# Optimization experiments

Measured on AMD Instinct MI355X. Metric: run time of the kernel, lower is better.

Reference implementation:

```python
import jax, jax.numpy as jnp
import numpy as np

B, C, H, W = 2, 128, 256, 256
E = 2                      # expan_att_chans
NUM_CHANS = 4
HEADS = NUM_CHANS * E      # 8
D = C // NUM_CHANS         # 32 head dim
EPS = 1e-12


def setup_inputs() -> dict:
    key = jax.random.key(0)
    ks = jax.random.split(key, 6)
    s = 0.05
    return {
        "x": jax.random.normal(ks[0], (B, C, H, W), jnp.float32),
        "w_qkv": jax.random.normal(ks[1], (C, 3 * E), jnp.float32) * s,   # groups=C, 1->3E per group
        "b_qkv": jax.random.normal(ks[2], (C, 3 * E), jnp.float32) * s,
        "w_fus": jax.random.normal(ks[3], (C, E), jnp.float32) * s,       # groups=C, E->1 per group
        "b_fus": jax.random.normal(ks[4], (C,), jnp.float32) * s,
        "t": jnp.ones((1, HEADS, 1, 1), jnp.float32),                     # learned temperature
    }


def _l2norm(a):
    n = jnp.sqrt(jnp.sum(a * a, axis=-1, keepdims=True))
    return a / jnp.maximum(n, EPS)


def reference(x, w_qkv, b_qkv, w_fus, b_fus, t):
    Bs, Cs, Hs, Ws = x.shape
    HW = Hs * Ws
    # grouped 1x1 conv (groups=C): each input channel -> 3E outputs
    qkv = jnp.einsum('bchw,ce->bechw', x, w_qkv) + b_qkv.T[None, :, :, None, None]
    # qkv: [B, 3E, C, H, W]; chunk into q,k,v along dim 1
    q, k, v = qkv[:, :E], qkv[:, E:2 * E], qkv[:, 2 * E:]
    # [B, E, C, H, W] -> [B, heads, d, HW]
    q = q.reshape(Bs, HEADS, D, HW)
    k = k.reshape(Bs, HEADS, D, HW)
    v = v.reshape(Bs, HEADS, D, HW)
    q = _l2norm(q)
    k = _l2norm(k)
    attn = jnp.einsum('bhdn,bhen->bhde', q, k) * t   # [B, heads, d, d]
    attn = jax.nn.softmax(attn, axis=-1)
    o = jnp.einsum('bhde,bhen->bhdn', attn, v)       # [B, heads, d, HW]
    # [B, heads, d, HW] -> [B, E, C, H, W] -> [B, C, E, H, W]
    o = o.reshape(Bs, E, Cs, Hs, Ws).transpose(0, 2, 1, 3, 4)
    # grouped 1x1 conv (groups=C): E inputs -> 1 output per channel
    out = jnp.einsum('bcehw,ce->bchw', o, w_fus) + b_fus[None, :, None, None]
    return out
```

## Files before the change

### kernel.cpp

```cpp
#include <hip/hip_runtime.h>
#include <hip/hip_bf16.h>
#include <cmath>

typedef __bf16 bf16_t;
typedef __attribute__((ext_vector_type(8)))  __bf16 bf16x8;
typedef __attribute__((ext_vector_type(16))) float  f32x16;
typedef __attribute__((ext_vector_type(4)))  float  f32x4;

#define HW    65536
#define BNC   8
#define CH    128
#define CBLK  128
#define FN    65536.0f
#define REPS  1e-12f

__device__ __forceinline__ bf16_t tob(float x){ return (bf16_t)x; }

__global__ __launch_bounds__(256) void k_gram(const float* __restrict__ x,
                                              float* __restrict__ P,
                                              float* __restrict__ PS)
{
    const int bid   = blockIdx.x;
    const int bnc   = bid >> 7;
    const int chunk = bid & (CH - 1);
    const int tid   = threadIdx.x;
    const int lane  = tid & 63;
    const int wv    = tid >> 6;
    const int ch    = lane & 31;
    const int hi    = lane >> 5;

    const float* px = x + ((size_t)(bnc * 32 + ch)) * HW
                        + chunk * (HW / CH) + wv * 128 + 8 * hi;

    f32x16 acc;
    #pragma unroll
    for (int r = 0; r < 16; ++r) acc[r] = 0.0f;
    float sx = 0.0f;

    #pragma unroll
    for (int s = 0; s < 8; ++s) {
        f32x4 u = *(const f32x4*)(px);
        f32x4 v = *(const f32x4*)(px + 4);
        px += 16;
        sx += (u.x + u.y + u.z + u.w) + (v.x + v.y + v.z + v.w);
        bf16x8 f;
        f[0]=tob(u.x); f[1]=tob(u.y); f[2]=tob(u.z); f[3]=tob(u.w);
        f[4]=tob(v.x); f[5]=tob(v.y); f[6]=tob(v.z); f[7]=tob(v.w);
        acc = __builtin_amdgcn_mfma_f32_32x32x16_bf16(f, f, acc, 0, 0, 0);
    }

    __shared__ float red[4][1024];
    __shared__ float sred[4][32];
    #pragma unroll
    for (int r = 0; r < 16; ++r) {
        int row = (r & 3) + 8 * (r >> 2) + 4 * hi;
        red[wv][row * 32 + ch] = acc[r];
    }
    sx += __shfl_xor(sx, 32);
    if (hi == 0) sred[wv][ch] = sx;
    __syncthreads();

    float* Pp = P + (size_t)bid * 1024;
    #pragma unroll
    for (int i = 0; i < 4; ++i) {
        int e = tid + 256 * i;
        Pp[e] = red[0][e] + red[1][e] + red[2][e] + red[3][e];
    }
    if (tid < 32)
        PS[bid * 32 + tid] = sred[0][tid] + sred[1][tid] + sred[2][tid] + sred[3][tid];
}

__global__ __launch_bounds__(1024) void k_attn(const float* __restrict__ P,
                                               const float* __restrict__ PS,
                                               const float* __restrict__ w_qkv,
                                               const float* __restrict__ b_qkv,
                                               const float* __restrict__ w_fus,
                                               const float* __restrict__ b_fus,
                                               const float* __restrict__ tin,
                                               float* __restrict__ M,
                                               float* __restrict__ K0)
{
    const int bnc = blockIdx.x;
    const int nc  = bnc & 3;
    const int tid = threadIdx.x;

    __shared__ float G[1024];
    __shared__ float Sx[32];

    {
        float g = 0.0f;
        const float* Pp = P + (size_t)bnc * CH * 1024;
        for (int c = 0; c < CH; ++c) g += Pp[c * 1024 + tid];
        G[tid] = g;
        if (tid < 32) {
            float s = 0.0f;
            const float* Sp = PS + bnc * CH * 32;
            for (int c = 0; c < CH; ++c) s += Sp[c * 32 + tid];
            Sx[tid] = s;
        }
    }
    __syncthreads();

    const int d = tid >> 5, j = tid & 31;
    const int cd = nc * 32 + d, cj = nc * 32 + j;
    const float Gdj = G[d * 32 + j], Gdd = G[d * 33], Gjj = G[j * 33];
    const float Sxd = Sx[d], Sxj = Sx[j];

    float mloc = 0.0f, kloc = 0.0f;
    #pragma unroll
    for (int e = 0; e < 2; ++e) {
        float aq = w_qkv[cd * 6 + e],     cq = b_qkv[cd * 6 + e];
        float ak = w_qkv[cj * 6 + 2 + e], ck = b_qkv[cj * 6 + 2 + e];
        float av = w_qkv[cj * 6 + 4 + e], cv = b_qkv[cj * 6 + 4 + e];
        float wf = w_fus[cd * 2 + e];
        float tv = tin[e * 4 + nc];

        float S  = aq * ak * Gdj + aq * ck * Sxd + cq * ak * Sxj + cq * ck * FN;
        float Nq = aq * aq * Gdd + 2.0f * aq * cq * Sxd + cq * cq * FN;
        float Nk = ak * ak * Gjj + 2.0f * ak * ck * Sxj + ck * ck * FN;
        float pre = S / (fmaxf(sqrtf(Nq), REPS) * fmaxf(sqrtf(Nk), REPS)) * tv;

        float mx = pre;
        #pragma unroll
        for (int o = 16; o; o >>= 1) mx = fmaxf(mx, __shfl_xor(mx, o));
        float p = expf(pre - mx);
        float sm = p;
        #pragma unroll
        for (int o = 16; o; o >>= 1) sm += __shfl_xor(sm, o);
        float A = p / sm;

        mloc += wf * A * av;
        kloc += wf * A * cv;
    }
    M[bnc * 1024 + d * 32 + j] = mloc;
    float kr = kloc;
    #pragma unroll
    for (int o = 16; o; o >>= 1) kr += __shfl_xor(kr, o);
    if (j == 0) K0[bnc * 32 + d] = b_fus[cd] + kr;
}

__global__ __launch_bounds__(256) void k_apply(const float* __restrict__ x,
                                               const float* __restrict__ M,
                                               const float* __restrict__ K0,
                                               float* __restrict__ out)
{
    const int bid = blockIdx.x;
    const int bnc = bid >> 7;
    const int blk = bid & (CBLK - 1);
    const int tid = threadIdx.x;
    const int lane = tid & 63;
    const int wv   = tid >> 6;
    const int rl   = lane & 31;
    const int hi   = lane >> 5;

    const float* Mp = M + bnc * 1024 + rl * 32;
    bf16x8 ma0, ma1;
    {
        f32x4 a = *(const f32x4*)(Mp + 8 * hi);
        f32x4 b = *(const f32x4*)(Mp + 8 * hi + 4);
        f32x4 c = *(const f32x4*)(Mp + 16 + 8 * hi);
        f32x4 d4 = *(const f32x4*)(Mp + 16 + 8 * hi + 4);
        ma0[0]=tob(a.x); ma0[1]=tob(a.y); ma0[2]=tob(a.z); ma0[3]=tob(a.w);
        ma0[4]=tob(b.x); ma0[5]=tob(b.y); ma0[6]=tob(b.z); ma0[7]=tob(b.w);
        ma1[0]=tob(c.x); ma1[1]=tob(c.y); ma1[2]=tob(c.z); ma1[3]=tob(c.w);
        ma1[4]=tob(d4.x); ma1[5]=tob(d4.y); ma1[6]=tob(d4.z); ma1[7]=tob(d4.w);
    }
    float k0r[16];
    #pragma unroll
    for (int r = 0; r < 16; ++r)
        k0r[r] = K0[bnc * 32 + (r & 3) + 8 * (r >> 2) + 4 * hi];

    const size_t xbase = (size_t)bnc * 32 * HW;
    const int p0 = blk * (HW / CBLK) + wv * 128;

    for (int c = 0; c < 4; ++c) {
        const int pxi = p0 + c * 32 + rl;
        const float* xp = x + xbase + pxi;
        bf16x8 xb0, xb1;
        #pragma unroll
        for (int j = 0; j < 8; ++j) {
            float v0 = xp[(size_t)(8 * hi + j) * HW];
            float v1 = xp[(size_t)(16 + 8 * hi + j) * HW];
            xb0[j] = tob(v0);
            xb1[j] = tob(v1);
        }
        f32x16 acc;
        #pragma unroll
        for (int r = 0; r < 16; ++r) acc[r] = k0r[r];
        acc = __builtin_amdgcn_mfma_f32_32x32x16_bf16(ma0, xb0, acc, 0, 0, 0);
        acc = __builtin_amdgcn_mfma_f32_32x32x16_bf16(ma1, xb1, acc, 0, 0, 0);

        float* op = out + xbase + pxi;
        #pragma unroll
        for (int r = 0; r < 16; ++r) {
            int row = (r & 3) + 8 * (r >> 2) + 4 * hi;
            op[(size_t)row * HW] = acc[r];
        }
    }
}

extern "C" void kernel_launch(void* const* d_in, const int* in_sizes, int n_in,
                              void* d_out, int out_size, void* d_ws, size_t ws_size,
                              hipStream_t stream)
{
    (void)in_sizes; (void)n_in; (void)out_size;
    const float* x      = (const float*)d_in[0];
    const float* w_qkv  = (const float*)d_in[1];
    const float* b_qkv  = (const float*)d_in[2];
    const float* w_fus  = (const float*)d_in[3];
    const float* b_fus  = (const float*)d_in[4];
    const float* tin    = (const float*)d_in[5];
    float* out = (float*)d_out;

    float* Mbuf  = (float*)d_ws;
    float* K0buf = Mbuf + BNC * 1024;
    const size_t small = (size_t)(BNC * 1024 + BNC * 32);
    const size_t needP  = (size_t)BNC * CH * 1024;
    const size_t needPS = (size_t)BNC * CH * 32;
    float *P, *PS;
    if (ws_size >= (small + needP + needPS) * sizeof(float)) {
        P  = K0buf + BNC * 32;
        PS = P + needP;
    } else {
        P  = out;
        PS = out + needP;
    }

    k_gram <<<BNC * CH,  256,  0, stream>>>(x, P, PS);
    k_attn <<<BNC,       1024, 0, stream>>>(P, PS, w_qkv, b_qkv, w_fus, b_fus, tin,
                                            Mbuf, K0buf);
    k_apply<<<BNC * CBLK, 256, 0, stream>>>(x, Mbuf, K0buf, out);
}
```

Baseline: 140.0 us.

## Stage gram tile in LDS and replace MFMA apply with coalesced FP32 FMA

k_gram now loads each 32x512 chunk of x with row-contiguous float4 reads, converts it to bf16 into a padded LDS tile, and computes the per-channel sums and the MFMA gram from LDS. Before, it used strided per-lane loads. k_apply drops the bf16 MFMA path and its strided scalar gather and scatter. Instead, each thread reads float4 of x for all 32 channels, accumulates a 32x32 FP32 matvec against a transposed M, and writes float4 results. This targets uncoalesced global access in both memory-bound kernels and removes bf16 rounding in apply. The cost is a large register footprint (128 accumulator floats), fewer apply blocks, and shared-memory atomics for the sums.

New measurement: 144.2 us. +3.0%, slower.

```diff
diff --git a/kernel.cpp b/kernel.cpp
--- a/kernel.cpp
+++ b/kernel.cpp
@@ -3,6 +3,7 @@
 #include <cmath>
 
 typedef __bf16 bf16_t;
+typedef __attribute__((ext_vector_type(4)))  __bf16 bf16x4;
 typedef __attribute__((ext_vector_type(8)))  __bf16 bf16x8;
 typedef __attribute__((ext_vector_type(16))) float  f32x16;
 typedef __attribute__((ext_vector_type(4)))  float  f32x4;
@@ -10,7 +11,7 @@
 #define HW    65536
 #define BNC   8
 #define CH    128
-#define CBLK  128
+#define APB   64
 #define FN    65536.0f
 #define REPS  1e-12f
 
@@ -20,6 +21,11 @@
                                               float* __restrict__ P,
                                               float* __restrict__ PS)
 {
+    __shared__ float smemf[8320];
+    __shared__ float sxl[32];
+    bf16_t (*tile)[520] = (bf16_t (*)[520])smemf;
+    float  (*red)[1024] = (float  (*)[1024])smemf;
+
     const int bid   = blockIdx.x;
     const int bnc   = bid >> 7;
     const int chunk = bid & (CH - 1);
@@ -29,35 +35,50 @@
     const int ch    = lane & 31;
     const int hi    = lane >> 5;
 
-    const float* px = x + ((size_t)(bnc * 32 + ch)) * HW
-                        + chunk * (HW / CH) + wv * 128 + 8 * hi;
+    if (tid < 32) sxl[tid] = 0.0f;
+    __syncthreads();
+
+    const float* xb = x + (size_t)bnc * 32 * HW + chunk * 512;
+    #pragma unroll
+    for (int it = 0; it < 16; ++it) {
+        int i   = tid + 256 * it;
+        int row = i >> 7;
+        int c4  = i & 127;
+        f32x4 v = *(const f32x4*)(xb + (size_t)row * HW + c4 * 4);
+        bf16x4 b;
+        b[0] = tob(v.x); b[1] = tob(v.y); b[2] = tob(v.z); b[3] = tob(v.w);
+        *(bf16x4*)&tile[row][c4 * 4] = b;
+    }
+    __syncthreads();
+
+    {
+        int sch = tid >> 3, seg = tid & 7;
+        float s = 0.0f;
+        #pragma unroll
+        for (int k8 = 0; k8 < 8; ++k8) {
+            bf16x8 u = *(const bf16x8*)&tile[sch][seg * 64 + k8 * 8];
+            #pragma unroll
+            for (int j = 0; j < 8; ++j) s += (float)u[j];
+        }
+        atomicAdd(&sxl[sch], s);
+    }
 
     f32x16 acc;
     #pragma unroll
     for (int r = 0; r < 16; ++r) acc[r] = 0.0f;
-    float sx = 0.0f;
-
-    #pragma unroll
-    for (int s = 0; s < 8; ++s) {
-        f32x4 u = *(const f32x4*)(px);
-        f32x4 v = *(const f32x4*)(px + 4);
-        px += 16;
-        sx += (u.x + u.y + u.z + u.w) + (v.x + v.y + v.z + v.w);
-        bf16x8 f;
-        f[0]=tob(u.x); f[1]=tob(u.y); f[2]=tob(u.z); f[3]=tob(u.w);
-        f[4]=tob(v.x); f[5]=tob(v.y); f[6]=tob(v.z); f[7]=tob(v.w);
+    #pragma unroll
+    for (int s8 = 0; s8 < 8; ++s8) {
+        int px = wv * 128 + s8 * 16 + 8 * hi;
+        bf16x8 f = *(const bf16x8*)&tile[ch][px];
         acc = __builtin_amdgcn_mfma_f32_32x32x16_bf16(f, f, acc, 0, 0, 0);
     }
-
-    __shared__ float red[4][1024];
-    __shared__ float sred[4][32];
+    __syncthreads();
+
     #pragma unroll
     for (int r = 0; r < 16; ++r) {
         int row = (r & 3) + 8 * (r >> 2) + 4 * hi;
         red[wv][row * 32 + ch] = acc[r];
     }
-    sx += __shfl_xor(sx, 32);
-    if (hi == 0) sred[wv][ch] = sx;
     __syncthreads();
 
     float* Pp = P + (size_t)bid * 1024;
@@ -66,8 +87,7 @@
         int e = tid + 256 * i;
         Pp[e] = red[0][e] + red[1][e] + red[2][e] + red[3][e];
     }
-    if (tid < 32)
-        PS[bid * 32 + tid] = sred[0][tid] + sred[1][tid] + sred[2][tid] + sred[3][tid];
+    if (tid < 32) PS[bid * 32 + tid] = sxl[tid];
 }
 
 __global__ __launch_bounds__(1024) void k_attn(const float* __restrict__ P,
@@ -77,7 +97,7 @@
                                                const float* __restrict__ w_fus,
                                                const float* __restrict__ b_fus,
                                                const float* __restrict__ tin,
-                                               float* __restrict__ M,
+                                               float* __restrict__ MT,
                                                float* __restrict__ K0)
 {
     const int bnc = blockIdx.x;
@@ -132,7 +152,7 @@
         mloc += wf * A * av;
         kloc += wf * A * cv;
     }
-    M[bnc * 1024 + d * 32 + j] = mloc;
+    MT[bnc * 1024 + j * 32 + d] = mloc;
     float kr = kloc;
     #pragma unroll
     for (int o = 16; o; o >>= 1) kr += __shfl_xor(kr, o);
@@ -140,62 +160,37 @@
 }
 
 __global__ __launch_bounds__(256) void k_apply(const float* __restrict__ x,
-                                               const float* __restrict__ M,
+                                               const float* __restrict__ MT,
                                                const float* __restrict__ K0,
                                                float* __restrict__ out)
 {
-    const int bid = blockIdx.x;
-    const int bnc = bid >> 7;
-    const int blk = bid & (CBLK - 1);
-    const int tid = threadIdx.x;
-    const int lane = tid & 63;
-    const int wv   = tid >> 6;
-    const int rl   = lane & 31;
-    const int hi   = lane >> 5;
-
-    const float* Mp = M + bnc * 1024 + rl * 32;
-    bf16x8 ma0, ma1;
-    {
-        f32x4 a = *(const f32x4*)(Mp + 8 * hi);
-        f32x4 b = *(const f32x4*)(Mp + 8 * hi + 4);
-        f32x4 c = *(const f32x4*)(Mp + 16 + 8 * hi);
-        f32x4 d4 = *(const f32x4*)(Mp + 16 + 8 * hi + 4);
-        ma0[0]=tob(a.x); ma0[1]=tob(a.y); ma0[2]=tob(a.z); ma0[3]=tob(a.w);
-        ma0[4]=tob(b.x); ma0[5]=tob(b.y); ma0[6]=tob(b.z); ma0[7]=tob(b.w);
-        ma1[0]=tob(c.x); ma1[1]=tob(c.y); ma1[2]=tob(c.z); ma1[3]=tob(c.w);
-        ma1[4]=tob(d4.x); ma1[5]=tob(d4.y); ma1[6]=tob(d4.z); ma1[7]=tob(d4.w);
-    }
-    float k0r[16];
-    #pragma unroll
-    for (int r = 0; r < 16; ++r)
-        k0r[r] = K0[bnc * 32 + (r & 3) + 8 * (r >> 2) + 4 * hi];
-
-    const size_t xbase = (size_t)bnc * 32 * HW;
-    const int p0 = blk * (HW / CBLK) + wv * 128;
-
-    for (int c = 0; c < 4; ++c) {
-        const int pxi = p0 + c * 32 + rl;
-        const float* xp = x + xbase + pxi;
-        bf16x8 xb0, xb1;
-        #pragma unroll
-        for (int j = 0; j < 8; ++j) {
-            float v0 = xp[(size_t)(8 * hi + j) * HW];
-            float v1 = xp[(size_t)(16 + 8 * hi + j) * HW];
-            xb0[j] = tob(v0);
-            xb1[j] = tob(v1);
+    const int bnc = blockIdx.x >> 6;
+    const int blk = blockIdx.x & (APB - 1);
+    const int p   = blk * 1024 + threadIdx.x * 4;
+
+    const float* xb = x   + (size_t)bnc * 32 * HW + p;
+    float*       ob = out + (size_t)bnc * 32 * HW + p;
+    const float* Mb = MT  + bnc * 1024;
+    const float* Kb = K0  + bnc * 32;
+
+    f32x4 acc[32];
+    const f32x4 zz = {0.0f, 0.0f, 0.0f, 0.0f};
+    #pragma unroll
+    for (int d = 0; d < 32; ++d) acc[d] = zz;
+
+    #pragma unroll 4
+    for (int e = 0; e < 32; ++e) {
+        f32x4 xv = *(const f32x4*)(xb + (size_t)e * HW);
+        #pragma unroll
+        for (int d = 0; d < 32; ++d) {
+            acc[d] += xv * Mb[e * 32 + d];
         }
-        f32x16 acc;
-        #pragma unroll
-        for (int r = 0; r < 16; ++r) acc[r] = k0r[r];
-        acc = __builtin_amdgcn_mfma_f32_32x32x16_bf16(ma0, xb0, acc, 0, 0, 0);
-        acc = __builtin_amdgcn_mfma_f32_32x32x16_bf16(ma1, xb1, acc, 0, 0, 0);
-
-        float* op = out + xbase + pxi;
-        #pragma unroll
-        for (int r = 0; r < 16; ++r) {
-            int row = (r & 3) + 8 * (r >> 2) + 4 * hi;
-            op[(size_t)row * HW] = acc[r];
-        }
+    }
+
+    #pragma unroll
+    for (int d = 0; d < 32; ++d) {
+        f32x4 r = acc[d] + Kb[d];
+        *(f32x4*)(ob + (size_t)d * HW) = r;
     }
 }
 
@@ -214,7 +209,7 @@
 
     float* Mbuf  = (float*)d_ws;
     float* K0buf = Mbuf + BNC * 1024;
-    const size_t small = (size_t)(BNC * 1024 + BNC * 32);
+    const size_t small  = (size_t)(BNC * 1024 + BNC * 32);
     const size_t needP  = (size_t)BNC * CH * 1024;
     const size_t needPS = (size_t)BNC * CH * 32;
     float *P, *PS;
@@ -229,5 +224,5 @@
     k_gram <<<BNC * CH,  256,  0, stream>>>(x, P, PS);
     k_attn <<<BNC,       1024, 0, stream>>>(P, PS, w_qkv, b_qkv, w_fus, b_fus, tin,
                                             Mbuf, K0buf);
-    k_apply<<<BNC * CBLK, 256, 0, stream>>>(x, Mbuf, K0buf, out);
-}
+    k_apply<<<BNC * APB, 256,  0, stream>>>(x, Mbuf, K0buf, out);
+}
```
